# Optimization experiments

Hardware: AMD Instinct MI355X
Metric: run time of the kernel (lower is better)

The kernel has to match this reference:

```python
import jax, jax.numpy as jnp
import numpy as np

B, H, W, C = 4, 64, 64, 256

def setup_inputs() -> dict:
    key = jax.random.key(0)
    k1, k2 = jax.random.split(key)
    xa = jax.random.normal(k1, (B, H, W, C), dtype=jnp.float32)
    xb = jax.random.normal(k2, (B, H, W, C), dtype=jnp.float32)
    gamma = jnp.float32(1.0)  # learned scalar (init 'zeros' in source; nonzero for testing)
    return {"xa": xa, "xb": xb, "gamma": gamma}


def _cross_branch(x_q, x_k, gamma):
    # x_q: source of queries, values, and residual; x_k: source of keys.
    b, h, w, c = x_q.shape
    q = x_q.reshape(b, h * w, c)            # [B,N,C]
    k = x_k.reshape(b, h * w, c)            # [B,N,C]
    energy = jnp.einsum('bnc,bmc->bnm', q, k)   # full N x N scores
    # softmax(max_row - energy) == softmax(-energy) (row max is shift-invariant)
    attention = jax.nn.softmax(-energy, axis=-1)
    out = jnp.einsum('bnm,bmc->bnc', attention, q)  # proj_value == reshaped x_q
    out = out.reshape(b, h, w, c)
    return gamma * out + x_q


def reference(xa, xb, gamma):
    out_a = _cross_branch(xa, xb, gamma)  # energya = Qa Kb^T, values/residual = xa
    out_b = _cross_branch(xb, xa, gamma)  # energyb = Qb Ka^T, values/residual = xb
    return (out_a, out_b)
```

## Files before the change

### kernel.cpp

```cpp
#include <hip/hip_runtime.h>
#include <hip/hip_bf16.h>
#include <stdint.h>

typedef _Float16 f16x8 __attribute__((ext_vector_type(8)));
typedef __fp16 fp16x2_t __attribute__((ext_vector_type(2)));
typedef float f32x4 __attribute__((ext_vector_type(4)));

#define MFMA_F16(A, B, C) __builtin_amdgcn_mfma_f32_16x16x32_f16(A, B, C, 0, 0, 0)
#define GLOAD_LDS16(g, l)                                                     \
    __builtin_amdgcn_global_load_lds(                                         \
        (const __attribute__((address_space(1))) void*)(g),                   \
        (__attribute__((address_space(3))) void*)(l), 16, 0, 0)

constexpr int Bb = 4, Nn = 4096, Cc = 256;
constexpr int BQ = 128;
constexpr int BK = 64;
constexpr int NT = Nn / BK;
constexpr int KPAD = 256;
constexpr int VPAD = 64;

constexpr size_t ASZ = (size_t)2 * Bb * Nn * Cc;
constexpr size_t WS_NEED = ASZ * 2 * 3;

__device__ __forceinline__ uint32_t pk16(float a, float b) {
    union { fp16x2_t h; uint32_t u; } cv;
    cv.h = __builtin_amdgcn_cvt_pkrtz(a, b);
    return cv.u;
}

__global__ __launch_bounds__(256)
void prep_kernel(const float* __restrict__ xa, const float* __restrict__ xb,
                 _Float16* __restrict__ hi, _Float16* __restrict__ lo,
                 _Float16* __restrict__ vt)
{
    const int n0 = blockIdx.x * 64, c0 = blockIdx.y * 64, ib = blockIdx.z;
    const float* x = ((ib >> 2) == 0 ? xa : xb) + (size_t)(ib & 3) * Nn * Cc;
    const size_t base = (size_t)ib * Nn * Cc;
    __shared__ ushort tile[64][68];
    const int t = threadIdx.x;
    const int r0 = t >> 4;
    const int c4 = (t & 15) * 4;
    #pragma unroll
    for (int ii = 0; ii < 4; ++ii) {
        const int r = r0 + ii * 16;
        float4 v = *(const float4*)&x[(size_t)(n0 + r) * Cc + c0 + c4];
        float vv[4] = {v.x, v.y, v.z, v.w};
        union { _Float16 h[4]; uint2 q; } H, L;
        #pragma unroll
        for (int e = 0; e < 4; ++e) {
            _Float16 h = (_Float16)vv[e];
            H.h[e] = h;
            L.h[e] = (_Float16)(vv[e] - (float)h);
        }
        *(uint2*)&hi[base + (size_t)(n0 + r) * Cc + c0 + c4] = H.q;
        *(uint2*)&lo[base + (size_t)(n0 + r) * Cc + c0 + c4] = L.q;
        *(uint2*)&tile[r][c4] = H.q;
    }
    __syncthreads();
    const int j4 = (t & 15) * 4;
    #pragma unroll
    for (int ii = 0; ii < 4; ++ii) {
        const int cr = r0 + ii * 16;
        ushort4 o;
        o.x = tile[j4 + 0][cr]; o.y = tile[j4 + 1][cr];
        o.z = tile[j4 + 2][cr]; o.w = tile[j4 + 3][cr];
        *(ushort4*)&vt[base + (size_t)(c0 + cr) * Nn + n0 + j4] = o;
    }
}

template<bool PREP>
__global__ __launch_bounds__(512, 1)
void attn_kernel(const float* __restrict__ xa, const float* __restrict__ xb,
                 const float* __restrict__ gamma_p, float* __restrict__ out,
                 const _Float16* __restrict__ hi, const _Float16* __restrict__ lo,
                 const _Float16* __restrict__ vt)
{
    const int bid = blockIdx.x;
    const int qtile = bid >> 3, b = bid & 3, dir = (bid >> 2) & 1;
    const float* qsrc = (dir == 0 ? xa : xb) + (size_t)b * Nn * Cc;
    const float* ksrc = (dir == 0 ? xb : xa) + (size_t)b * Nn * Cc;
    float* outp = out + (size_t)dir * Bb * Nn * Cc + (size_t)b * Nn * Cc;
    const int qib = dir * Bb + b;
    const int kib = (dir ^ 1) * Bb + b;
    const _Float16* qhiB = hi + (size_t)qib * Nn * Cc;
    const _Float16* qloB = lo + (size_t)qib * Nn * Cc;
    const _Float16* kB   = hi + (size_t)kib * Nn * Cc;
    const _Float16* vtB  = vt + (size_t)qib * Nn * Cc;

    __shared__ _Float16 sK[2][BK][KPAD];
    __shared__ _Float16 sVt[2][Cc][VPAD];

    const int t = threadIdx.x, lane = t & 63, w = t >> 6;
    const int l15 = lane & 15, g = lane >> 4;
    const int khalf = g * 8;
    const int rsw = (l15 & 7) << 3;

    f16x8 qhi[8], qlo[8];
    const int qrow = qtile * BQ + w * 16 + l15;
    if constexpr (PREP) {
        #pragma unroll
        for (int j = 0; j < 8; ++j) {
            union { uint4 u; f16x8 h; } A, C2;
            A.u  = *(const uint4*)(qhiB + (size_t)qrow * Cc + j * 32 + khalf);
            C2.u = *(const uint4*)(qloB + (size_t)qrow * Cc + j * 32 + khalf);
            A.u.x ^= 0x80008000u; A.u.y ^= 0x80008000u; A.u.z ^= 0x80008000u; A.u.w ^= 0x80008000u;
            C2.u.x ^= 0x80008000u; C2.u.y ^= 0x80008000u; C2.u.z ^= 0x80008000u; C2.u.w ^= 0x80008000u;
            qhi[j] = A.h; qlo[j] = C2.h;
        }
    } else {
        const float* qb = qsrc + (size_t)qrow * Cc;
        #pragma unroll
        for (int j = 0; j < 8; ++j) {
            float4 v0 = *(const float4*)(qb + j * 32 + khalf);
            float4 v1 = *(const float4*)(qb + j * 32 + khalf + 4);
            float xv[8] = {v0.x, v0.y, v0.z, v0.w, v1.x, v1.y, v1.z, v1.w};
            #pragma unroll
            for (int e = 0; e < 8; ++e) {
                float xn = -xv[e];
                _Float16 h = (_Float16)xn;
                qhi[j][e] = h;
                qlo[j][e] = (_Float16)(xn - (float)h);
            }
        }
    }

    f32x4 O[16];
    #pragma unroll
    for (int i = 0; i < 16; ++i) O[i] = (f32x4){0.f, 0.f, 0.f, 0.f};
    float mrow = -INFINITY;
    float lsum = 0.f;

    const int krow0 = w * 8;
    const int klsub = lane >> 5;
    int offK[4];
    #pragma unroll
    for (int i = 0; i < 4; ++i) {
        const int rsub = i * 2 + klsub;
        const int sc = ((lane & 31) * 8) ^ ((rsub & 7) << 3);
        offK[i] = (krow0 + rsub) * Cc + sc;
    }
    const int vrow0 = w * 32;
    const int vlsub = lane >> 3;
    const int vcol  = ((lane & 7) * 8) ^ ((vlsub & 7) << 3);
    int offV[4];
    #pragma unroll
    for (int i = 0; i < 4; ++i)
        offV[i] = (vrow0 + i * 8 + vlsub) * Nn + vcol;

    auto stage = [&](int bufi, int m0) {
        #pragma unroll
        for (int i = 0; i < 4; ++i)
            GLOAD_LDS16(kB + (size_t)m0 * Cc + offK[i], &sK[bufi][krow0 + i * 2][0]);
        #pragma unroll
        for (int i = 0; i < 4; ++i)
            GLOAD_LDS16(vtB + (size_t)m0 + offV[i], &sVt[bufi][vrow0 + i * 8][0]);
    };

    auto compute = [&](int cur) {
        f32x4 S[4];
        #pragma unroll
        for (int s = 0; s < 4; ++s) S[s] = (f32x4){0.f, 0.f, 0.f, 0.f};
        __builtin_amdgcn_s_setprio(1);
        #pragma unroll
        for (int j = 0; j < 8; ++j) {
            const int ko = j * 32 + khalf;
            f16x8 k0 = *(const f16x8*)&sK[cur][l15][ko ^ rsw];
            f16x8 k1 = *(const f16x8*)&sK[cur][16 + l15][ko ^ rsw];
            f16x8 k2 = *(const f16x8*)&sK[cur][32 + l15][ko ^ rsw];
            f16x8 k3 = *(const f16x8*)&sK[cur][48 + l15][ko ^ rsw];
            S[0] = MFMA_F16(k0, qhi[j], S[0]);
            S[1] = MFMA_F16(k1, qhi[j], S[1]);
            S[2] = MFMA_F16(k2, qhi[j], S[2]);
            S[3] = MFMA_F16(k3, qhi[j], S[3]);
            S[0] = MFMA_F16(k0, qlo[j], S[0]);
            S[1] = MFMA_F16(k1, qlo[j], S[1]);
            S[2] = MFMA_F16(k2, qlo[j], S[2]);
            S[3] = MFMA_F16(k3, qlo[j], S[3]);
        }
        __builtin_amdgcn_s_setprio(0);

        float tm = fmaxf(fmaxf(fmaxf(S[0][0], S[0][1]), fmaxf(S[0][2], S[0][3])),
                         fmaxf(fmaxf(S[1][0], S[1][1]), fmaxf(S[1][2], S[1][3])));
        tm = fmaxf(tm, fmaxf(fmaxf(fmaxf(S[2][0], S[2][1]), fmaxf(S[2][2], S[2][3])),
                             fmaxf(fmaxf(S[3][0], S[3][1]), fmaxf(S[3][2], S[3][3]))));
        tm = fmaxf(tm, __shfl_xor(tm, 16, 64));
        tm = fmaxf(tm, __shfl_xor(tm, 32, 64));
        const bool need = tm > mrow + 8.f;
        if (__any(need)) {
            float mn = fmaxf(mrow, tm);
            float a = __expf(mrow - mn);
            mrow = mn;
            lsum *= a;
            const int base = lane & 48;
            const int g4 = (g & 3) * 4;
            float a0 = __shfl(a, base | (g4 + 0), 64);
            float a1 = __shfl(a, base | (g4 + 1), 64);
            float a2 = __shfl(a, base | (g4 + 2), 64);
            float a3 = __shfl(a, base | (g4 + 3), 64);
            #pragma unroll
            for (int i = 0; i < 16; ++i) {
                O[i][0] *= a0; O[i][1] *= a1; O[i][2] *= a2; O[i][3] *= a3;
            }
        }

        uint32_t P2[4][2];
        float ps = 0.f;
        #pragma unroll
        for (int s = 0; s < 4; ++s) {
            float p0 = __expf(S[s][0] - mrow);
            float p1 = __expf(S[s][1] - mrow);
            float p2 = __expf(S[s][2] - mrow);
            float p3 = __expf(S[s][3] - mrow);
            ps += (p0 + p1) + (p2 + p3);
            P2[s][0] = pk16(p0, p1);
            P2[s][1] = pk16(p2, p3);
        }
        lsum += ps;

        uint32_t q00 = __shfl_xor(P2[0][0], 16, 64);
        uint32_t q01 = __shfl_xor(P2[0][1], 16, 64);
        uint32_t q10 = __shfl_xor(P2[1][0], 16, 64);
        uint32_t q11 = __shfl_xor(P2[1][1], 16, 64);
        uint32_t q20 = __shfl_xor(P2[2][0], 16, 64);
        uint32_t q21 = __shfl_xor(P2[2][1], 16, 64);
        uint32_t q30 = __shfl_xor(P2[3][0], 16, 64);
        uint32_t q31 = __shfl_xor(P2[3][1], 16, 64);
        const bool low = (g < 2);
        const bool odd = (g & 1);
        uint32_t m0_ = low ? P2[1][0] : P2[0][0];
        uint32_t m1_ = low ? P2[1][1] : P2[0][1];
        uint32_t m2_ = low ? P2[3][0] : P2[2][0];
        uint32_t m3_ = low ? P2[3][1] : P2[2][1];
        uint32_t p0_ = low ? q10 : q00;
        uint32_t p1_ = low ? q11 : q01;
        uint32_t p2_ = low ? q30 : q20;
        uint32_t p3_ = low ? q31 : q21;
        uint32_t sl0 = odd ? p0_ : m0_, sh0 = odd ? m0_ : p0_;
        uint32_t sl1 = odd ? p1_ : m1_, sh1 = odd ? m1_ : p1_;
        uint32_t sl2 = odd ? p2_ : m2_, sh2 = odd ? m2_ : p2_;
        uint32_t sl3 = odd ? p3_ : m3_, sh3 = odd ? m3_ : p3_;
        uint32_t R0 = __shfl_xor(sl0, 32, 64);
        uint32_t R1 = __shfl_xor(sl1, 32, 64);
        uint32_t R2 = __shfl_xor(sl2, 32, 64);
        uint32_t R3 = __shfl_xor(sl3, 32, 64);
        uint32_t R4 = __shfl_xor(sh0, 32, 64);
        uint32_t R5 = __shfl_xor(sh1, 32, 64);
        uint32_t R6 = __shfl_xor(sh2, 32, 64);
        uint32_t R7 = __shfl_xor(sh3, 32, 64);
        uint32_t A0 = (g == 0) ? P2[0][0] : ((g == 3) ? q10 : R0);
        uint32_t A1 = (g == 0) ? P2[0][1] : ((g == 3) ? q11 : R1);
        uint32_t A2 = (g == 0) ? P2[2][0] : ((g == 3) ? q30 : R2);
        uint32_t A3 = (g == 0) ? P2[2][1] : ((g == 3) ? q31 : R3);
        uint32_t B0 = (g == 0) ? q00 : ((g == 3) ? P2[1][0] : R4);
        uint32_t B1 = (g == 0) ? q01 : ((g == 3) ? P2[1][1] : R5);
        uint32_t B2 = (g == 0) ? q20 : ((g == 3) ? P2[3][0] : R6);
        uint32_t B3 = (g == 0) ? q21 : ((g == 3) ? P2[3][1] : R7);
        union { uint32_t u[4]; f16x8 h; } U0, U1;
        U0.u[0] = A0; U0.u[1] = A1; U0.u[2] = B0; U0.u[3] = B1;
        U1.u[0] = A2; U1.u[1] = A3; U1.u[2] = B2; U1.u[3] = B3;
        f16x8 pa0 = U0.h, pa1 = U1.h;

        __builtin_amdgcn_s_setprio(1);
        #pragma unroll
        for (int i = 0; i < 16; ++i) {
            f16x8 vb0 = *(const f16x8*)&sVt[cur][i * 16 + l15][khalf ^ rsw];
            f16x8 vb1 = *(const f16x8*)&sVt[cur][i * 16 + l15][(32 + khalf) ^ rsw];
            O[i] = MFMA_F16(pa0, vb0, O[i]);
            O[i] = MFMA_F16(pa1, vb1, O[i]);
        }
        __builtin_amdgcn_s_setprio(0);
    };

    if constexpr (PREP) {
        stage(0, 0);
        __syncthreads();
        for (int ti = 0; ti < NT; ++ti) {
            if (ti + 1 < NT) stage((ti & 1) ^ 1, (ti + 1) * BK);
            compute(ti & 1);
            __syncthreads();
        }
    } else {
        const int fr = t & 63, fc = (t >> 6) * 32;
        const int fsw = (fr & 7) << 3;
        for (int ti = 0; ti < NT; ++ti) {
            const int m0 = ti * BK;
            __syncthreads();
            #pragma unroll
            for (int e = 0; e < 32; e += 4) {
                float4 kv = *(const float4*)&ksrc[(size_t)(m0 + fr) * Cc + fc + e];
                sK[0][fr][(fc + e + 0) ^ fsw] = (_Float16)kv.x;
                sK[0][fr][(fc + e + 1) ^ fsw] = (_Float16)kv.y;
                sK[0][fr][(fc + e + 2) ^ fsw] = (_Float16)kv.z;
                sK[0][fr][(fc + e + 3) ^ fsw] = (_Float16)kv.w;
                float4 xv = *(const float4*)&qsrc[(size_t)(m0 + fr) * Cc + fc + e];
                sVt[0][fc + e + 0][fr ^ (((fc + e + 0) & 7) << 3)] = (_Float16)xv.x;
                sVt[0][fc + e + 1][fr ^ (((fc + e + 1) & 7) << 3)] = (_Float16)xv.y;
                sVt[0][fc + e + 2][fr ^ (((fc + e + 2) & 7) << 3)] = (_Float16)xv.z;
                sVt[0][fc + e + 3][fr ^ (((fc + e + 3) & 7) << 3)] = (_Float16)xv.w;
            }
            __syncthreads();
            compute(0);
        }
    }

    float lv = lsum;
    lv += __shfl_xor(lv, 16, 64);
    lv += __shfl_xor(lv, 32, 64);
    const float gma = gamma_p[0];
    const int base = lane & 48;
    const int g4 = (g & 3) * 4;
    #pragma unroll
    for (int r = 0; r < 4; ++r) {
        const float lvr = __shfl(lv, base | (g4 + r), 64);
        const float inv = 1.f / lvr;
        const int row = qtile * BQ + w * 16 + g4 + r;
        const size_t ro = (size_t)row * Cc + l15;
        #pragma unroll
        for (int i = 0; i < 16; ++i) {
            float o = O[i][r] * inv;
            outp[ro + i * 16] = gma * o + qsrc[ro + i * 16];
        }
    }
}

extern "C" void kernel_launch(void* const* d_in, const int* in_sizes, int n_in,
                              void* d_out, int out_size, void* d_ws, size_t ws_size,
                              hipStream_t stream) {
    (void)in_sizes; (void)n_in; (void)out_size;
    const float* xa = (const float*)d_in[0];
    const float* xb = (const float*)d_in[1];
    const float* gm = (const float*)d_in[2];
    float* out = (float*)d_out;

    dim3 agrid(256);
    if (ws_size >= WS_NEED) {
        _Float16* hi = (_Float16*)d_ws;
        _Float16* lo = hi + ASZ;
        _Float16* vt = lo + ASZ;
        prep_kernel<<<dim3(Nn / 64, Cc / 64, 2 * Bb), 256, 0, stream>>>(xa, xb, hi, lo, vt);
        attn_kernel<true><<<agrid, 512, 0, stream>>>(xa, xb, gm, out, hi, lo, vt);
    } else {
        attn_kernel<false><<<agrid, 512, 0, stream>>>(xa, xb, gm, out, nullptr, nullptr, nullptr);
    }
}
```

Measured before the change: 218.4 us.

## Software-pipeline QK^T of next tile against PV of current tile

Splits the per-tile work into separate QK^T, softmax and PV stages. The loop now issues the next tile's QK^T before the current tile's PV, and prefetches K two tiles ahead. V gets a third LDS buffer so the async global-to-LDS loads do not collide with buffers still being read. The intent is to overlap MFMA work and memory latency across iterations and to break the serial dependence of softmax on QK^T. It also splits the PV MFMA loop into two passes over the V halves. In exchange, LDS use grows to about 160KB and register pressure rises because S and the P fragments stay live across stages.

```diff
diff --git a/kernel.cpp b/kernel.cpp
--- a/kernel.cpp
+++ b/kernel.cpp
@@ -88,7 +88,7 @@
     const _Float16* vtB  = vt + (size_t)qib * Nn * Cc;
 
     __shared__ _Float16 sK[2][BK][KPAD];
-    __shared__ _Float16 sVt[2][Cc][VPAD];
+    __shared__ _Float16 sVt[3][Cc][VPAD];
 
     const int t = threadIdx.x, lane = t & 63, w = t >> 6;
     const int l15 = lane & 15, g = lane >> 4;
@@ -130,6 +130,9 @@
     float mrow = -INFINITY;
     float lsum = 0.f;
 
+    f32x4 S[4];
+    f16x8 pa0, pa1;
+
     const int krow0 = w * 8;
     const int klsub = lane >> 5;
     int offK[4];
@@ -147,27 +150,28 @@
     for (int i = 0; i < 4; ++i)
         offV[i] = (vrow0 + i * 8 + vlsub) * Nn + vcol;
 
-    auto stage = [&](int bufi, int m0) {
+    auto stageK = [&](int bufi, int m0) {
         #pragma unroll
         for (int i = 0; i < 4; ++i)
             GLOAD_LDS16(kB + (size_t)m0 * Cc + offK[i], &sK[bufi][krow0 + i * 2][0]);
+    };
+    auto stageV = [&](int vbi, int m0) {
         #pragma unroll
         for (int i = 0; i < 4; ++i)
-            GLOAD_LDS16(vtB + (size_t)m0 + offV[i], &sVt[bufi][vrow0 + i * 8][0]);
-    };
-
-    auto compute = [&](int cur) {
-        f32x4 S[4];
+            GLOAD_LDS16(vtB + (size_t)m0 + offV[i], &sVt[vbi][vrow0 + i * 8][0]);
+    };
+
+    auto qkt = [&](int kb) {
         #pragma unroll
         for (int s = 0; s < 4; ++s) S[s] = (f32x4){0.f, 0.f, 0.f, 0.f};
         __builtin_amdgcn_s_setprio(1);
         #pragma unroll
         for (int j = 0; j < 8; ++j) {
             const int ko = j * 32 + khalf;
-            f16x8 k0 = *(const f16x8*)&sK[cur][l15][ko ^ rsw];
-            f16x8 k1 = *(const f16x8*)&sK[cur][16 + l15][ko ^ rsw];
-            f16x8 k2 = *(const f16x8*)&sK[cur][32 + l15][ko ^ rsw];
-            f16x8 k3 = *(const f16x8*)&sK[cur][48 + l15][ko ^ rsw];
+            f16x8 k0 = *(const f16x8*)&sK[kb][l15][ko ^ rsw];
+            f16x8 k1 = *(const f16x8*)&sK[kb][16 + l15][ko ^ rsw];
+            f16x8 k2 = *(const f16x8*)&sK[kb][32 + l15][ko ^ rsw];
+            f16x8 k3 = *(const f16x8*)&sK[kb][48 + l15][ko ^ rsw];
             S[0] = MFMA_F16(k0, qhi[j], S[0]);
             S[1] = MFMA_F16(k1, qhi[j], S[1]);
             S[2] = MFMA_F16(k2, qhi[j], S[2]);
@@ -178,7 +182,9 @@
             S[3] = MFMA_F16(k3, qlo[j], S[3]);
         }
         __builtin_amdgcn_s_setprio(0);
-
+    };
+
+    auto softmax = [&]() {
         float tm = fmaxf(fmaxf(fmaxf(S[0][0], S[0][1]), fmaxf(S[0][2], S[0][3])),
                          fmaxf(fmaxf(S[1][0], S[1][1]), fmaxf(S[1][2], S[1][3])));
         tm = fmaxf(tm, fmaxf(fmaxf(fmaxf(S[2][0], S[2][1]), fmaxf(S[2][2], S[2][3])),
@@ -202,7 +208,6 @@
                 O[i][0] *= a0; O[i][1] *= a1; O[i][2] *= a2; O[i][3] *= a3;
             }
         }
-
         uint32_t P2[4][2];
         float ps = 0.f;
         #pragma unroll
@@ -216,7 +221,6 @@
             P2[s][1] = pk16(p2, p3);
         }
         lsum += ps;
-
         uint32_t q00 = __shfl_xor(P2[0][0], 16, 64);
         uint32_t q01 = __shfl_xor(P2[0][1], 16, 64);
         uint32_t q10 = __shfl_xor(P2[1][0], 16, 64);
@@ -258,26 +262,39 @@
         union { uint32_t u[4]; f16x8 h; } U0, U1;
         U0.u[0] = A0; U0.u[1] = A1; U0.u[2] = B0; U0.u[3] = B1;
         U1.u[0] = A2; U1.u[1] = A3; U1.u[2] = B2; U1.u[3] = B3;
-        f16x8 pa0 = U0.h, pa1 = U1.h;
-
+        pa0 = U0.h; pa1 = U1.h;
+    };
+
+    auto pv = [&](int vb) {
         __builtin_amdgcn_s_setprio(1);
         #pragma unroll
         for (int i = 0; i < 16; ++i) {
-            f16x8 vb0 = *(const f16x8*)&sVt[cur][i * 16 + l15][khalf ^ rsw];
-            f16x8 vb1 = *(const f16x8*)&sVt[cur][i * 16 + l15][(32 + khalf) ^ rsw];
+            f16x8 vb0 = *(const f16x8*)&sVt[vb][i * 16 + l15][khalf ^ rsw];
             O[i] = MFMA_F16(pa0, vb0, O[i]);
+        }
+        #pragma unroll
+        for (int i = 0; i < 16; ++i) {
+            f16x8 vb1 = *(const f16x8*)&sVt[vb][i * 16 + l15][(32 + khalf) ^ rsw];
             O[i] = MFMA_F16(pa1, vb1, O[i]);
         }
         __builtin_amdgcn_s_setprio(0);
     };
 
     if constexpr (PREP) {
-        stage(0, 0);
+        stageK(0, 0); stageV(0, 0);
         __syncthreads();
+        stageK(1, BK); stageV(1, BK);
+        qkt(0);
+        softmax();
         for (int ti = 0; ti < NT; ++ti) {
-            if (ti + 1 < NT) stage((ti & 1) ^ 1, (ti + 1) * BK);
-            compute(ti & 1);
             __syncthreads();
+            if (ti + 1 < NT) qkt((ti + 1) & 1);
+            if (ti + 2 < NT) {
+                stageK(ti & 1, (ti + 2) * BK);
+                stageV((ti + 2) % 3, (ti + 2) * BK);
+            }
+            pv(ti % 3);
+            if (ti + 1 < NT) softmax();
         }
     } else {
         const int fr = t & 63, fc = (t >> 6) * 32;
@@ -299,7 +316,9 @@
                 sVt[0][fc + e + 3][fr ^ (((fc + e + 3) & 7) << 3)] = (_Float16)xv.w;
             }
             __syncthreads();
-            compute(0);
+            qkt(0);
+            softmax();
+            pv(0);
         }
     }
 
```

After: 208.7 us, median of 2. 4.5% less time.
